# Optimization experiments

Hardware: AMD Instinct MI355X
Metric: run time of the kernel (lower is better)

Reference implementation:

```python
import jax, jax.numpy as jnp
import numpy as np

DIM = 1024
HEADS = 16
DIM_HEAD = 64
INNER = HEADS * DIM_HEAD  # 1024
SCALE = DIM_HEAD ** -0.5


def setup_inputs() -> dict:
    key = jax.random.key(0)
    k0, k1, k2 = jax.random.split(key, 3)
    x = jax.random.normal(k0, (4, 2048, DIM), dtype=jnp.float32)
    ln_gamma = jnp.ones((DIM,), dtype=jnp.float32)
    ln_beta = jnp.zeros((DIM,), dtype=jnp.float32)
    w_qkv = jax.random.normal(k1, (DIM, 3 * INNER), dtype=jnp.float32) * (DIM ** -0.5)
    w_out = jax.random.normal(k2, (INNER, DIM), dtype=jnp.float32) * (INNER ** -0.5)
    b_out = jnp.zeros((DIM,), dtype=jnp.float32)
    return {"x": x, "ln_gamma": ln_gamma, "ln_beta": ln_beta,
            "w_qkv": w_qkv, "w_out": w_out, "b_out": b_out}


def reference(x, ln_gamma, ln_beta, w_qkv, w_out, b_out):
    # LayerNorm over last dim (eps matches torch default 1e-5)
    mu = jnp.mean(x, axis=-1, keepdims=True)
    var = jnp.mean(jnp.square(x - mu), axis=-1, keepdims=True)
    xn = (x - mu) * jax.lax.rsqrt(var + 1e-5) * ln_gamma + ln_beta
    # QKV projection (no bias)
    qkv = xn @ w_qkv  # [b, t, 3*inner]
    q, k, v = jnp.split(qkv, 3, axis=-1)
    B, T, _ = x.shape
    def to_heads(t):
        return t.reshape(B, T, HEADS, DIM_HEAD).transpose(0, 2, 1, 3)  # b h t d
    q, k, v = to_heads(q), to_heads(k), to_heads(v)
    dots = jnp.einsum('bhid,bhjd->bhij', q, k) * SCALE
    attn = jax.nn.softmax(dots, axis=-1)
    out = jnp.einsum('bhij,bhjd->bhid', attn, v)
    out = out.transpose(0, 2, 1, 3).reshape(B, T, INNER)
    return out @ w_out + b_out
```

## Files before the change

kernel.cpp:

```cpp
#include <hip/hip_runtime.h>


#define DIMX 1024
#define TSEQ 2048
#define NB 4
#define NH 16
#define DH 64
#define NROWS (NB * TSEQ)
#define QSCALE 0.18033688011112042f

typedef __bf16 bf16_t;
typedef __bf16 bf16x8 __attribute__((ext_vector_type(8)));
typedef __bf16 bf16x4 __attribute__((ext_vector_type(4)));
typedef float f32x4 __attribute__((ext_vector_type(4)));

#if __has_builtin(__builtin_amdgcn_exp2f)
#define EXP2F __builtin_amdgcn_exp2f
#else
#define EXP2F exp2f
#endif

__device__ __forceinline__ bf16x4 cvt4(f32x4 v) {
    return __builtin_convertvector(v, bf16x4);
}
__device__ __forceinline__ void async16(const bf16_t* g, bf16_t* l) {
    __builtin_amdgcn_global_load_lds(
        (const __attribute__((address_space(1))) unsigned int*)g,
        (__attribute__((address_space(3))) unsigned int*)l, 16, 0, 0);
}

__global__ __launch_bounds__(256) void ln_kernel(
    const float* __restrict__ x, const float* __restrict__ g,
    const float* __restrict__ b, bf16_t* __restrict__ xn) {
    int row = blockIdx.x, tid = threadIdx.x;
    const float4 xv = *(const float4*)(x + (size_t)row * DIMX + tid * 4);
    float s = xv.x + xv.y + xv.z + xv.w;
    float q = xv.x * xv.x + xv.y * xv.y + xv.z * xv.z + xv.w * xv.w;
    for (int o = 32; o > 0; o >>= 1) {
        s += __shfl_xor(s, o);
        q += __shfl_xor(q, o);
    }
    __shared__ float2 red[4];
    int wave = tid >> 6, lane = tid & 63;
    if (lane == 0) red[wave] = make_float2(s, q);
    __syncthreads();
    float2 r0 = red[0], r1 = red[1], r2 = red[2], r3 = red[3];
    s = r0.x + r1.x + r2.x + r3.x;
    q = r0.y + r1.y + r2.y + r3.y;
    float mu = s * (1.0f / DIMX);
    float var = q * (1.0f / DIMX) - mu * mu;
    float rstd = rsqrtf(var + 1e-5f);
    float4 gv = *(const float4*)(g + tid * 4);
    float4 bv = *(const float4*)(b + tid * 4);
    f32x4 r;
    r[0] = (xv.x - mu) * rstd * gv.x + bv.x;
    r[1] = (xv.y - mu) * rstd * gv.y + bv.y;
    r[2] = (xv.z - mu) * rstd * gv.z + bv.z;
    r[3] = (xv.w - mu) * rstd * gv.w + bv.w;
    *(bf16x4*)(xn + (size_t)row * DIMX + tid * 4) = cvt4(r);
}

__global__ __launch_bounds__(256) void transpose_cast(
    const float* __restrict__ src, bf16_t* __restrict__ dst, int R, int C) {
    __shared__ float tile[32][33];
    int c0 = blockIdx.x * 32, r0 = blockIdx.y * 32;
    int tx = threadIdx.x, ty = threadIdx.y;
    for (int i = ty; i < 32; i += 8)
        tile[i][tx] = src[(size_t)(r0 + i) * C + c0 + tx];
    __syncthreads();
    for (int i = ty; i < 32; i += 8)
        dst[(size_t)(c0 + i) * R + r0 + tx] = (bf16_t)tile[tx][i];
}

#define MFMA16 __builtin_amdgcn_mfma_f32_16x16x32_bf16

template <int MODE>
__global__ __launch_bounds__(512, 2) void gemm256(
    const bf16_t* __restrict__ A, const bf16_t* __restrict__ BT,
    void* __restrict__ Cout, const float* __restrict__ bias, int M, int N, int K) {
    __shared__ __align__(16) bf16_t As[2][256 * 64];
    __shared__ __align__(16) bf16_t Bs[2][256 * 64];
    int tid = threadIdx.x, lane = tid & 63, wave = tid >> 6;
    int lm = lane & 15, quad = lane >> 4;
    int wr = wave >> 2, wc = wave & 3;

    int nbx = gridDim.x;
    int nwg = nbx * gridDim.y;
    int linear = blockIdx.y * nbx + blockIdx.x;
    int cpx = nwg >> 3;
    int swz = (linear & 7) * cpx + (linear >> 3);
    int bx = swz % nbx, by = swz / nbx;
    int m0 = by * 256, n0 = bx * 256;

    int srow = tid >> 3, sc8 = tid & 7;
    int scol = (sc8 ^ (srow & 7)) << 3;
    const bf16_t* ga = A + (size_t)(m0 + srow) * K + scol;
    const bf16_t* gb = BT + (size_t)(n0 + srow) * K + scol;
    int ldst = tid << 3;

    int sw0 = ((quad ^ (lm & 7)) << 3);
    int sw1 = (((4 + quad) ^ (lm & 7)) << 3);

    f32x4 zero = {0.f, 0.f, 0.f, 0.f};
    f32x4 acc[8][4];
#pragma unroll
    for (int i = 0; i < 8; ++i)
#pragma unroll
        for (int j = 0; j < 4; ++j) acc[i][j] = zero;

#pragma unroll
    for (int i = 0; i < 4; ++i) async16(ga + (size_t)i * 64 * K, &As[0][i * 4096 + ldst]);
#pragma unroll
    for (int i = 0; i < 4; ++i) async16(gb + (size_t)i * 64 * K, &Bs[0][i * 4096 + ldst]);
    asm volatile("s_waitcnt vmcnt(0)" ::: "memory");
    __builtin_amdgcn_s_barrier();

    int nkt = K >> 6;
    for (int kt = 0; kt < nkt; ++kt) {
        int c = kt & 1;
        int k1 = (kt + 1) << 6;
        bool pf = (kt + 1) < nkt;
        const bf16_t* pa = &As[c][0];
        const bf16_t* pb = &Bs[c][0];
        bf16_t* na = &As[c ^ 1][0];
        bf16_t* nb = &Bs[c ^ 1][0];
        bf16x8 af[4][2], bfr[2][2];

#pragma unroll
        for (int t = 0; t < 4; ++t) {
            int ro = (wr * 128 + t * 16 + lm) * 64;
            af[t][0] = *(const bf16x8*)&pa[ro + sw0];
            af[t][1] = *(const bf16x8*)&pa[ro + sw1];
        }
#pragma unroll
        for (int t = 0; t < 2; ++t) {
            int ro = (wc * 64 + t * 16 + lm) * 64;
            bfr[t][0] = *(const bf16x8*)&pb[ro + sw0];
            bfr[t][1] = *(const bf16x8*)&pb[ro + sw1];
        }
        if (pf) {
#pragma unroll
            for (int i = 0; i < 4; ++i)
                async16(ga + (size_t)i * 64 * K + k1, &na[i * 4096 + ldst]);
        }
        __builtin_amdgcn_s_barrier();
        asm volatile("s_waitcnt lgkmcnt(0)" ::: "memory");
        __builtin_amdgcn_s_setprio(1);
#pragma unroll
        for (int mt = 0; mt < 4; ++mt)
#pragma unroll
            for (int nt = 0; nt < 2; ++nt) {
                acc[mt][nt] = MFMA16(af[mt][0], bfr[nt][0], acc[mt][nt], 0, 0, 0);
                acc[mt][nt] = MFMA16(af[mt][1], bfr[nt][1], acc[mt][nt], 0, 0, 0);
            }
        __builtin_amdgcn_s_setprio(0);
        __builtin_amdgcn_s_barrier();

#pragma unroll
        for (int t = 0; t < 2; ++t) {
            int ro = (wc * 64 + (2 + t) * 16 + lm) * 64;
            bfr[t][0] = *(const bf16x8*)&pb[ro + sw0];
            bfr[t][1] = *(const bf16x8*)&pb[ro + sw1];
        }
        if (pf) {
#pragma unroll
            for (int i = 0; i < 4; ++i)
                async16(gb + (size_t)i * 64 * K + k1, &nb[i * 4096 + ldst]);
        }
        __builtin_amdgcn_s_barrier();
        asm volatile("s_waitcnt lgkmcnt(0)" ::: "memory");
        __builtin_amdgcn_s_setprio(1);
#pragma unroll
        for (int mt = 0; mt < 4; ++mt)
#pragma unroll
            for (int nt = 0; nt < 2; ++nt) {
                acc[mt][2 + nt] = MFMA16(af[mt][0], bfr[nt][0], acc[mt][2 + nt], 0, 0, 0);
                acc[mt][2 + nt] = MFMA16(af[mt][1], bfr[nt][1], acc[mt][2 + nt], 0, 0, 0);
            }
        __builtin_amdgcn_s_setprio(0);
        __builtin_amdgcn_s_barrier();

#pragma unroll
        for (int t = 0; t < 4; ++t) {
            int ro = (wr * 128 + (4 + t) * 16 + lm) * 64;
            af[t][0] = *(const bf16x8*)&pa[ro + sw0];
            af[t][1] = *(const bf16x8*)&pa[ro + sw1];
        }
        __builtin_amdgcn_s_barrier();
        asm volatile("s_waitcnt lgkmcnt(0)" ::: "memory");
        __builtin_amdgcn_s_setprio(1);
#pragma unroll
        for (int mt = 0; mt < 4; ++mt)
#pragma unroll
            for (int nt = 0; nt < 2; ++nt) {
                acc[4 + mt][2 + nt] = MFMA16(af[mt][0], bfr[nt][0], acc[4 + mt][2 + nt], 0, 0, 0);
                acc[4 + mt][2 + nt] = MFMA16(af[mt][1], bfr[nt][1], acc[4 + mt][2 + nt], 0, 0, 0);
            }
        __builtin_amdgcn_s_setprio(0);
        __builtin_amdgcn_s_barrier();

#pragma unroll
        for (int t = 0; t < 2; ++t) {
            int ro = (wc * 64 + t * 16 + lm) * 64;
            bfr[t][0] = *(const bf16x8*)&pb[ro + sw0];
            bfr[t][1] = *(const bf16x8*)&pb[ro + sw1];
        }
        __builtin_amdgcn_s_barrier();
        asm volatile("s_waitcnt lgkmcnt(0)" ::: "memory");
        __builtin_amdgcn_s_setprio(1);
#pragma unroll
        for (int mt = 0; mt < 4; ++mt)
#pragma unroll
            for (int nt = 0; nt < 2; ++nt) {
                acc[4 + mt][nt] = MFMA16(af[mt][0], bfr[nt][0], acc[4 + mt][nt], 0, 0, 0);
                acc[4 + mt][nt] = MFMA16(af[mt][1], bfr[nt][1], acc[4 + mt][nt], 0, 0, 0);
            }
        __builtin_amdgcn_s_setprio(0);
        asm volatile("s_waitcnt vmcnt(0)" ::: "memory");
        __builtin_amdgcn_s_barrier();
    }

#pragma unroll
    for (int mt = 0; mt < 8; ++mt) {
#pragma unroll
        for (int nt = 0; nt < 4; ++nt) {
            int m = m0 + wr * 128 + mt * 16 + quad * 4;
            int n = n0 + wc * 64 + nt * 16 + lm;
            if (MODE == 1) {
                int sel = n >> 10, nn = n & 1023, h = nn >> 6, d = nn & 63;
                int b = m >> 11, t = m & 2047;
                if (sel == 2) {
                    *(bf16x4*)((bf16_t*)Cout + (size_t)2 * 8388608 +
                               ((size_t)((b * NH + h) * DH + d)) * TSEQ + t) = cvt4(acc[mt][nt]);
                } else {
                    f32x4 sv = acc[mt][nt] * (sel == 0 ? QSCALE : 1.0f);
                    bf16x4 c4 = cvt4(sv);
#pragma unroll
                    for (int r = 0; r < 4; ++r)
                        ((bf16_t*)Cout)[(size_t)sel * 8388608 +
                                        ((size_t)((b * NH + h) * TSEQ + t + r)) * DH + d] = c4[r];
                }
            } else {
                float bn = bias[n];
#pragma unroll
                for (int r = 0; r < 4; ++r)
                    ((float*)Cout)[(size_t)(m + r) * N + n] = acc[mt][nt][r] + bn;
            }
        }
    }
}

__global__ __launch_bounds__(256, 2) void attn_mfma(
    const bf16_t* __restrict__ qkv, bf16_t* __restrict__ o) {
    int bh = blockIdx.y;
    int qt = blockIdx.x;
    const bf16_t* qb = qkv + (size_t)bh * TSEQ * DH;
    const bf16_t* kb = qkv + (size_t)8388608 + (size_t)bh * TSEQ * DH;
    const bf16_t* vb = qkv + (size_t)16777216 + (size_t)bh * DH * TSEQ;
    int tid = threadIdx.x, wave = tid >> 6, lane = tid & 63;
    int lm = lane & 15, quad = lane >> 4, lx = lm & 7;

    __shared__ __align__(16) bf16_t Ks[64 * 64];
    __shared__ __align__(16) bf16_t Vt[64 * 64];
    __shared__ __align__(16) bf16_t Ps[4 * 1024];

    int roff = tid >> 3;
    int cperm = ((tid & 7) ^ (roff & 7)) * 8;
    const bf16_t* kp0 = kb + (size_t)roff * DH + cperm;
    const bf16_t* kp1 = kb + (size_t)(32 + roff) * DH + cperm;
    const bf16_t* vp0 = vb + (size_t)roff * TSEQ + cperm;
    const bf16_t* vp1 = vb + (size_t)(32 + roff) * TSEQ + cperm;
    bf16_t* lk0 = &Ks[tid * 8];
    bf16_t* lk1 = &Ks[(256 + tid) * 8];
    bf16_t* lv0 = &Vt[tid * 8];
    bf16_t* lv1 = &Vt[(256 + tid) * 8];

    bf16x8 qf[4][2];
#pragma unroll
    for (int u = 0; u < 4; ++u)
#pragma unroll
        for (int ks = 0; ks < 2; ++ks)
            qf[u][ks] = *(const bf16x8*)(qb +
                (size_t)(qt * 256 + wave * 64 + u * 16 + lm) * DH + ks * 32 + quad * 8);

    f32x4 zero = {0.f, 0.f, 0.f, 0.f};
    f32x4 m16 = {-16.f, -16.f, -16.f, -16.f};
    f32x4 acc[4][4];
#pragma unroll
    for (int u = 0; u < 4; ++u)
#pragma unroll
        for (int dt = 0; dt < 4; ++dt) acc[u][dt] = zero;
    f32x4 l4[4] = {zero, zero, zero, zero};

    int fo0 = (quad ^ lx) * 8;
    int fo1 = ((4 + quad) ^ lx) * 8;
    int pb = wave * 1024 + lm * 64;

    for (int jt = 0; jt < TSEQ / 64; ++jt) {
        __syncthreads();
        async16(kp0, lk0);
        async16(kp1, lk1);
        async16(vp0, lv0);
        async16(vp1, lv1);
        kp0 += 64 * DH; kp1 += 64 * DH; vp0 += 64; vp1 += 64;
        __syncthreads();

        bf16x8 kf[4][2];
#pragma unroll
        for (int nt = 0; nt < 4; ++nt) {
            kf[nt][0] = *(const bf16x8*)&Ks[(nt * 16 + lm) * 64 + fo0];
            kf[nt][1] = *(const bf16x8*)&Ks[(nt * 16 + lm) * 64 + fo1];
        }

        bf16x8 pf[4][2];
#pragma unroll
        for (int u = 0; u < 4; ++u) {
            f32x4 s[4];
#pragma unroll
            for (int nt = 0; nt < 4; ++nt) {
                s[nt] = __builtin_amdgcn_mfma_f32_16x16x32_bf16(kf[nt][0], qf[u][0], m16, 0, 0, 0);
                s[nt] = __builtin_amdgcn_mfma_f32_16x16x32_bf16(kf[nt][1], qf[u][1], s[nt], 0, 0, 0);
            }
#pragma unroll
            for (int nt = 0; nt < 4; ++nt) {
                f32x4 p;
#pragma unroll
                for (int e = 0; e < 4; ++e) p[e] = EXP2F(s[nt][e]);
                l4[u] += p;
                *(bf16x4*)&Ps[pb + ((nt * 2 + (quad >> 1)) ^ lx) * 8 + (quad & 1) * 4] = cvt4(p);
            }
            pf[u][0] = *(const bf16x8*)&Ps[pb + fo0];
            pf[u][1] = *(const bf16x8*)&Ps[pb + fo1];
        }

#pragma unroll
        for (int dt = 0; dt < 4; ++dt) {
            bf16x8 vf0 = *(const bf16x8*)&Vt[(dt * 16 + lm) * 64 + fo0];
            bf16x8 vf1 = *(const bf16x8*)&Vt[(dt * 16 + lm) * 64 + fo1];
#pragma unroll
            for (int u = 0; u < 4; ++u) {
                acc[u][dt] = __builtin_amdgcn_mfma_f32_16x16x32_bf16(vf0, pf[u][0], acc[u][dt], 0, 0, 0);
                acc[u][dt] = __builtin_amdgcn_mfma_f32_16x16x32_bf16(vf1, pf[u][1], acc[u][dt], 0, 0, 0);
            }
        }
    }

    int b = bh >> 4, h = bh & 15;
#pragma unroll
    for (int u = 0; u < 4; ++u) {
        float l = (l4[u][0] + l4[u][1]) + (l4[u][2] + l4[u][3]);
        l += __shfl_xor(l, 16);
        l += __shfl_xor(l, 32);
        float rl = 1.0f / l;
        int t = qt * 256 + wave * 64 + u * 16 + lm;
#pragma unroll
        for (int dt = 0; dt < 4; ++dt) {
            f32x4 ov = acc[u][dt] * rl;
            *(bf16x4*)(o + ((size_t)(b * TSEQ + t)) * DIMX + h * DH + dt * 16 + quad * 4) = cvt4(ov);
        }
    }
}

extern "C" void kernel_launch(void* const* d_in, const int* in_sizes, int n_in,
                              void* d_out, int out_size, void* d_ws, size_t ws_size,
                              hipStream_t stream) {
    const float* x = (const float*)d_in[0];
    const float* g = (const float*)d_in[1];
    const float* be = (const float*)d_in[2];
    const float* w_qkv = (const float*)d_in[3];
    const float* w_out = (const float*)d_in[4];
    const float* b_out = (const float*)d_in[5];
    float* out = (float*)d_out;
    char* ws = (char*)d_ws;

    bf16_t* xn = (bf16_t*)(ws);
    bf16_t* wqkvT = (bf16_t*)(ws + 16777216);
    bf16_t* woutT = (bf16_t*)(ws + 23068672);
    bf16_t* qkv = (bf16_t*)(ws + 25165824);
    bf16_t* attno = (bf16_t*)(ws + 75497472);

    ln_kernel<<<NROWS, 256, 0, stream>>>(x, g, be, xn);
    transpose_cast<<<dim3(96, 32), dim3(32, 8), 0, stream>>>(w_qkv, wqkvT, 1024, 3072);
    transpose_cast<<<dim3(32, 32), dim3(32, 8), 0, stream>>>(w_out, woutT, 1024, 1024);
    gemm256<1><<<dim3(12, 32), 512, 0, stream>>>(xn, wqkvT, (void*)qkv, nullptr, NROWS, 3072, 1024);
    attn_mfma<<<dim3(8, 64), 256, 0, stream>>>(qkv, attno);
    gemm256<2><<<dim3(4, 32), 512, 0, stream>>>(attno, woutT, (void*)out, b_out, NROWS, 1024, 1024);
}
```

Before: 287.3 us.

## Double-buffer K/V tiles in attention kernel to overlap loads with MFMA

Splits the K and V shared-memory tiles into two buffers and issues the async global-to-LDS copy of the next tile before computing on the current one. Each iteration ends with one waitcnt plus barrier instead of two syncthreads around the load. The goal is to hide global-load latency behind the QK and PV MFMA work. It costs an extra 16 KB of LDS per block, which could limit occupancy at two blocks per CU.

```diff
diff --git a/kernel.cpp b/kernel.cpp
--- a/kernel.cpp
+++ b/kernel.cpp
@@ -260,8 +260,8 @@
     int tid = threadIdx.x, wave = tid >> 6, lane = tid & 63;
     int lm = lane & 15, quad = lane >> 4, lx = lm & 7;
 
-    __shared__ __align__(16) bf16_t Ks[64 * 64];
-    __shared__ __align__(16) bf16_t Vt[64 * 64];
+    __shared__ __align__(16) bf16_t Ks[2][64 * 64];
+    __shared__ __align__(16) bf16_t Vt[2][64 * 64];
     __shared__ __align__(16) bf16_t Ps[4 * 1024];
 
     int roff = tid >> 3;
@@ -270,10 +270,7 @@
     const bf16_t* kp1 = kb + (size_t)(32 + roff) * DH + cperm;
     const bf16_t* vp0 = vb + (size_t)roff * TSEQ + cperm;
     const bf16_t* vp1 = vb + (size_t)(32 + roff) * TSEQ + cperm;
-    bf16_t* lk0 = &Ks[tid * 8];
-    bf16_t* lk1 = &Ks[(256 + tid) * 8];
-    bf16_t* lv0 = &Vt[tid * 8];
-    bf16_t* lv1 = &Vt[(256 + tid) * 8];
+    int l0 = tid * 8, l1 = (256 + tid) * 8;
 
     bf16x8 qf[4][2];
 #pragma unroll
@@ -296,20 +293,29 @@
     int fo1 = ((4 + quad) ^ lx) * 8;
     int pb = wave * 1024 + lm * 64;
 
+    async16(kp0, &Ks[0][l0]);
+    async16(kp1, &Ks[0][l1]);
+    async16(vp0, &Vt[0][l0]);
+    async16(vp1, &Vt[0][l1]);
+    kp0 += 64 * DH; kp1 += 64 * DH; vp0 += 64; vp1 += 64;
+    asm volatile("s_waitcnt vmcnt(0)" ::: "memory");
+    __builtin_amdgcn_s_barrier();
+
     for (int jt = 0; jt < TSEQ / 64; ++jt) {
-        __syncthreads();
-        async16(kp0, lk0);
-        async16(kp1, lk1);
-        async16(vp0, lv0);
-        async16(vp1, lv1);
-        kp0 += 64 * DH; kp1 += 64 * DH; vp0 += 64; vp1 += 64;
-        __syncthreads();
+        int c = jt & 1;
+        if (jt + 1 < TSEQ / 64) {
+            async16(kp0, &Ks[c ^ 1][l0]);
+            async16(kp1, &Ks[c ^ 1][l1]);
+            async16(vp0, &Vt[c ^ 1][l0]);
+            async16(vp1, &Vt[c ^ 1][l1]);
+            kp0 += 64 * DH; kp1 += 64 * DH; vp0 += 64; vp1 += 64;
+        }
 
         bf16x8 kf[4][2];
 #pragma unroll
         for (int nt = 0; nt < 4; ++nt) {
-            kf[nt][0] = *(const bf16x8*)&Ks[(nt * 16 + lm) * 64 + fo0];
-            kf[nt][1] = *(const bf16x8*)&Ks[(nt * 16 + lm) * 64 + fo1];
+            kf[nt][0] = *(const bf16x8*)&Ks[c][(nt * 16 + lm) * 64 + fo0];
+            kf[nt][1] = *(const bf16x8*)&Ks[c][(nt * 16 + lm) * 64 + fo1];
         }
 
         bf16x8 pf[4][2];
@@ -335,14 +341,17 @@
 
 #pragma unroll
         for (int dt = 0; dt < 4; ++dt) {
-            bf16x8 vf0 = *(const bf16x8*)&Vt[(dt * 16 + lm) * 64 + fo0];
-            bf16x8 vf1 = *(const bf16x8*)&Vt[(dt * 16 + lm) * 64 + fo1];
+            bf16x8 vf0 = *(const bf16x8*)&Vt[c][(dt * 16 + lm) * 64 + fo0];
+            bf16x8 vf1 = *(const bf16x8*)&Vt[c][(dt * 16 + lm) * 64 + fo1];
 #pragma unroll
             for (int u = 0; u < 4; ++u) {
                 acc[u][dt] = __builtin_amdgcn_mfma_f32_16x16x32_bf16(vf0, pf[u][0], acc[u][dt], 0, 0, 0);
                 acc[u][dt] = __builtin_amdgcn_mfma_f32_16x16x32_bf16(vf1, pf[u][1], acc[u][dt], 0, 0, 0);
             }
         }
+
+        asm volatile("s_waitcnt vmcnt(0)" ::: "memory");
+        __builtin_amdgcn_s_barrier();
     }
 
     int b = bh >> 4, h = bh & 15;
```

Result: no change. 286.0 us (-0.4%).
